# Kernel optimization log

Hardware: AMD Instinct MI355X
Metric: run time of the kernel (lower is better)

Reference implementation:

```python
import jax, jax.numpy as jnp
import numpy as np

NUM_GRAPHS = 128
EPS = 1e-5


def _instance_norm(x, seg, num_seg):
    # Per-graph instance norm over rows grouped by seg (PyG InstanceNorm, affine=False).
    ones = jnp.ones((x.shape[0], 1), x.dtype)
    cnt = jnp.maximum(jax.ops.segment_sum(ones, seg, num_segments=num_seg), 1.0)  # [G,1]
    mean = jax.ops.segment_sum(x, seg, num_segments=num_seg) / cnt               # [G,C]
    xc = x - mean[seg]
    var = jax.ops.segment_sum(xc * xc, seg, num_segments=num_seg) / cnt          # [G,C]
    return xc * jax.lax.rsqrt(var[seg] + EPS)


def setup_inputs() -> dict:
    key = jax.random.key(0)
    ks = jax.random.split(key, 8)
    N, E, H, G = 50000, 800000, 64, NUM_GRAPHS
    emb = jax.random.normal(ks[0], (N, H), dtype=jnp.float32)
    edge_index = jax.random.randint(ks[1], (2, E), 0, N, dtype=jnp.int64)
    batch = jnp.sort(jax.random.randint(ks[2], (N,), 0, G, dtype=jnp.int64))
    s1 = 1.0 / np.sqrt(2 * H)
    s2 = 1.0 / np.sqrt(4 * H)
    s3 = 1.0 / np.sqrt(H)
    return {
        "emb": emb,
        "edge_index": edge_index,
        "batch": batch,
        "W1": jax.random.normal(ks[3], (2 * H, 4 * H), dtype=jnp.float32) * s1,
        "b1": jnp.zeros((4 * H,), jnp.float32),
        "W2": jax.random.normal(ks[4], (4 * H, H), dtype=jnp.float32) * s2,
        "b2": jnp.zeros((H,), jnp.float32),
        "W3": jax.random.normal(ks[5], (H, 1), dtype=jnp.float32) * s3,
        "b3": jnp.zeros((1,), jnp.float32),
    }


def reference(emb, edge_index, batch, W1, b1, W2, b2, W3, b3):
    col, row = edge_index[0], edge_index[1]
    # Gather both endpoint embeddings and concat: [E, 2H]
    f12 = jnp.concatenate([emb[col], emb[row]], axis=-1)
    seg = batch[col]  # graph id per edge
    # MLP([2H, 4H, H, 1]): Linear -> InstanceNorm(batch) -> ReLU (dropout=identity in eval)
    h = jnp.maximum(_instance_norm(f12 @ W1 + b1, seg, NUM_GRAPHS), 0.0)
    h = jnp.maximum(_instance_norm(h @ W2 + b2, seg, NUM_GRAPHS), 0.0)
    att_log_logits = h @ W3 + b3  # [E, 1]
    return att_log_logits
```

## Files before the change

kernel.cpp:

```cpp
#include <hip/hip_runtime.h>
#include <hip/hip_bf16.h>
#include <stdint.h>

#define NG 128
#define EPSI 1e-5f

typedef __attribute__((ext_vector_type(8))) __bf16 bf16x8;
typedef __attribute__((ext_vector_type(4))) float f32x4;

union ABFrag { bf16x8 v; unsigned short u[8]; uint4 q; };
union U8 { uint4 q; unsigned short u[8]; };

__device__ __forceinline__ float b2f(unsigned short u){
  union { unsigned int i; float f; } v; v.i = ((unsigned int)u) << 16; return v.f;
}
__device__ __forceinline__ unsigned short f2b(float f){
  union { float f; unsigned int i; } v; v.f = f;
  unsigned int r = v.i + 0x7fffu + ((v.i >> 16) & 1u);
  return (unsigned short)(r >> 16);
}
__device__ __forceinline__ unsigned int pk2(float lo, float hi){
  unsigned int r;
  asm("v_cvt_pk_bf16_f32 %0, %1, %2" : "=v"(r) : "v"(lo), "v"(hi));
  return r;
}

__global__ void kprep(const float* __restrict__ emb, const float* __restrict__ W1,
                      const float* __restrict__ W2,
                      const int* __restrict__ ei, const int* __restrict__ batch,
                      unsigned short* __restrict__ embb, unsigned short* __restrict__ WcF,
                      unsigned short* __restrict__ W2F, unsigned int* __restrict__ hist,
                      unsigned int* __restrict__ nodeh, int N, int E){
  __shared__ unsigned int h[NG];
  for (int i = threadIdx.x; i < NG; i += 256) h[i] = 0;
  __syncthreads();
  int idx = blockIdx.x * 256 + threadIdx.x;
  int stride = gridDim.x * 256;
  int embCnt4 = N * 16;
  for (int i = idx; i < embCnt4; i += stride){
    float4 v = *(const float4*)(emb + (size_t)i * 4);
    ushort4 o; o.x = f2b(v.x); o.y = f2b(v.y); o.z = f2b(v.z); o.w = f2b(v.w);
    *(ushort4*)(embb + (size_t)i * 4) = o;
  }
  for (int i = idx; i < 32 * 2 * 64 * 8; i += stride){
    int j = i & 7, lane = (i >> 3) & 63, ks = (i >> 9) & 1, tn = i >> 10;
    int quad = lane >> 4, l15 = lane & 15;
    int k = ks * 32 + quad * 8 + j;
    int n = tn * 16 + l15;
    float wv = (n < 256) ? W1[k * 256 + n] : W1[(k + 64) * 256 + (n - 256)];
    WcF[i] = f2b(wv);
  }
  for (int i = idx; i < 4 * 8 * 64 * 8; i += stride){
    int j = i & 7, lane = (i >> 3) & 63, ks = (i >> 9) & 7, w = i >> 12;
    int quad = lane >> 4, l15 = lane & 15;
    W2F[i] = f2b(W2[(ks * 32 + quad * 8 + j) * 64 + w * 16 + l15]);
  }
  for (int e = idx; e < E; e += stride){
    int cn = ei[e];
    atomicAdd(&h[batch[cn]], 1u);
    atomicAdd(&nodeh[cn], 1u);
  }
  __syncthreads();
  for (int i = threadIdx.x; i < NG; i += 256)
    if (h[i]) atomicAdd(&hist[i], h[i]);
}

__global__ void __launch_bounds__(256) kscan(const unsigned int* __restrict__ nodeh,
                      const unsigned int* __restrict__ hist,
                      const int* __restrict__ batch,
                      unsigned int* __restrict__ ncursor,
                      unsigned int* __restrict__ gmeta, int N){
  __shared__ unsigned int sh[3];
  __shared__ unsigned int wtot[4];
  int g = blockIdx.x;
  int t = threadIdx.x;
  unsigned int part = 0;
  for (int i = t; i < g; i += 256) part += (hist[i] + 31u) & ~31u;
  #pragma unroll
  for (int d = 1; d < 64; d <<= 1) part += __shfl_xor(part, d);
  if ((t & 63) == 0) wtot[t >> 6] = part;
  if (t == 64 || t == 65){
    int target = g + (t - 64);
    int lo = 0, hi = N;
    while (lo < hi){ int mid = (lo + hi) >> 1; if (batch[mid] < target) lo = mid + 1; else hi = mid; }
    sh[1 + (t - 64)] = lo;
  }
  __syncthreads();
  if (t == 0){
    unsigned int pb = wtot[0] + wtot[1] + wtot[2] + wtot[3];
    sh[0] = pb;
    gmeta[g] = pb;
    if (g == NG - 1) gmeta[NG] = pb + ((hist[g] + 31u) & ~31u);
  }
  __syncthreads();
  unsigned int run = sh[0];
  int lo = (int)sh[1], hi = (int)sh[2];
  int wid = t >> 6;
  for (int base = lo; base < hi; base += 256){
    int i = base + t;
    unsigned int v = (i < hi) ? nodeh[i] : 0u;
    unsigned int x = v;
    #pragma unroll
    for (int d = 1; d < 64; d <<= 1){
      unsigned int y = __shfl_up(x, d);
      if ((t & 63) >= d) x += y;
    }
    if ((t & 63) == 63) wtot[wid] = x;
    __syncthreads();
    unsigned int woff = 0;
    #pragma unroll
    for (int wb = 0; wb < 4; ++wb) if (wb < wid) woff += wtot[wb];
    if (i < hi) ncursor[i] = run + woff + x - v;
    run += wtot[0] + wtot[1] + wtot[2] + wtot[3];
    __syncthreads();
  }
}

__global__ void kscatter(const int* __restrict__ ei, const int* __restrict__ batch, int E,
                         unsigned int* __restrict__ ncursor, int4* __restrict__ einfo){
  int idx = blockIdx.x * 256 + threadIdx.x;
  for (int e = idx; e < E; e += gridDim.x * 256){
    int cn = ei[e], rn = ei[E + e];
    int g = batch[cn];
    unsigned int p = atomicAdd(&ncursor[cn], 1u);
    einfo[p] = make_int4(cn, rn, g, e);
  }
}

__global__ void kpad(int4* __restrict__ einfo, const unsigned int* __restrict__ hist,
                     const unsigned int* __restrict__ gmeta){
  int g = blockIdx.x;
  unsigned int cnt = hist[g];
  if (!cnt) return;
  unsigned int pe = (cnt + 31u) & ~31u;
  if (cnt == pe) return;
  unsigned int base = gmeta[g];
  int4 e0 = einfo[base]; e0.w = -1;
  for (unsigned int i = cnt + threadIdx.x; i < pe; i += 64)
    einfo[base + i] = e0;
}

__global__ void __launch_bounds__(256) kgemm1(const unsigned short* __restrict__ embb,
    const unsigned short* __restrict__ WcF, const float* __restrict__ b1,
    unsigned short* __restrict__ PQb, int Nn){
  int wave = threadIdx.x >> 6, lane = threadIdx.x & 63;
  int quad = lane >> 4, l15 = lane & 15;
  int tm = blockIdx.x * 4 + wave;
  int tmmax = (Nn + 15) >> 4;
  if (tm >= tmmax) return;
  int m = tm * 16 + l15; if (m >= Nn) m = Nn - 1;
  ABFrag a0, a1;
  a0.q = *(const uint4*)(embb + (size_t)m * 64 + quad * 8);
  a1.q = *(const uint4*)(embb + (size_t)m * 64 + 32 + quad * 8);
  int rowbase = tm * 16 + quad * 4;
  #pragma unroll 4
  for (int tn = 0; tn < 32; ++tn){
    ABFrag b0, b1f;
    b0.q  = *(const uint4*)(WcF + ((size_t)(tn * 2 + 0) * 64 + lane) * 8);
    b1f.q = *(const uint4*)(WcF + ((size_t)(tn * 2 + 1) * 64 + lane) * 8);
    f32x4 acc = {0.f, 0.f, 0.f, 0.f};
    acc = __builtin_amdgcn_mfma_f32_16x16x32_bf16(a0.v, b0.v, acc, 0, 0, 0);
    acc = __builtin_amdgcn_mfma_f32_16x16x32_bf16(a1.v, b1f.v, acc, 0, 0, 0);
    int col = tn * 16 + l15;
    float bias = (col < 256) ? b1[col] : 0.0f;
    #pragma unroll
    for (int r = 0; r < 4; ++r){
      int rowg = rowbase + r;
      if (rowg < Nn) PQb[(size_t)rowg * 512 + col] = f2b(acc[r] + bias);
    }
  }
}

__global__ void __launch_bounds__(256) kstats1(const unsigned short* __restrict__ PQb,
                        const int4* __restrict__ einfo, const unsigned int* __restrict__ gmeta,
                        float* __restrict__ sum1, float* __restrict__ sq1){
  __shared__ float lsum[8][256];
  __shared__ float lsq[8][256];
  int tid = threadIdx.x;
  int EP = (int)gmeta[NG];
  int i0 = blockIdx.x * 512;
  if (i0 >= EP) return;
  for (int i = tid; i < 8 * 256; i += 256){ ((float*)lsum)[i] = 0.f; ((float*)lsq)[i] = 0.f; }
  __syncthreads();
  int i1 = min(EP, i0 + 512);
  int gfirst = einfo[i0].z;
  int eo = tid >> 5;
  int c8 = (tid & 31) * 8;
  float s[8], q[8];
  #pragma unroll
  for (int t = 0; t < 8; ++t){ s[t] = 0.f; q[t] = 0.f; }
  int cur = -1;
  auto flushreg = [&](){
    if (cur >= 0){
      unsigned slot = (unsigned)(cur - gfirst);
      if (slot < 8u){
        #pragma unroll
        for (int t = 0; t < 8; ++t){
          atomicAdd(&lsum[slot][c8 + t], s[t]);
          atomicAdd(&lsq[slot][c8 + t], q[t]);
        }
      } else {
        #pragma unroll
        for (int t = 0; t < 8; ++t){
          atomicAdd(&sum1[cur * 256 + c8 + t], s[t]);
          atomicAdd(&sq1[cur * 256 + c8 + t], q[t]);
        }
      }
      #pragma unroll
      for (int t = 0; t < 8; ++t){ s[t] = 0.f; q[t] = 0.f; }
    }
  };
  auto accum = [&](const U8& pu, const U8& qu){
    #pragma unroll
    for (int t = 0; t < 8; ++t){
      float y = b2f(pu.u[t]) + b2f(qu.u[t]);
      s[t] += y; q[t] += y * y;
    }
  };
  for (int p = i0 + eo; p < i1; p += 32){
    int4 ev0 = einfo[p];
    int pa = p + 8, pb = p + 16, pc = p + 24;
    int4 ev1 = (pa < i1) ? einfo[pa] : make_int4(0, 0, -1, -1);
    int4 ev2 = (pb < i1) ? einfo[pb] : make_int4(0, 0, -1, -1);
    int4 ev3 = (pc < i1) ? einfo[pc] : make_int4(0, 0, -1, -1);
    U8 pu0, qu0, pu1, qu1, pu2, qu2, pu3, qu3;
    pu0.q = *(const uint4*)(PQb + (size_t)ev0.x * 512 + c8);
    qu0.q = *(const uint4*)(PQb + (size_t)ev0.y * 512 + 256 + c8);
    pu1.q = *(const uint4*)(PQb + (size_t)ev1.x * 512 + c8);
    qu1.q = *(const uint4*)(PQb + (size_t)ev1.y * 512 + 256 + c8);
    pu2.q = *(const uint4*)(PQb + (size_t)ev2.x * 512 + c8);
    qu2.q = *(const uint4*)(PQb + (size_t)ev2.y * 512 + 256 + c8);
    pu3.q = *(const uint4*)(PQb + (size_t)ev3.x * 512 + c8);
    qu3.q = *(const uint4*)(PQb + (size_t)ev3.y * 512 + 256 + c8);
    if (ev0.z != cur){ flushreg(); cur = ev0.z; }
    if (ev0.w >= 0) accum(pu0, qu0);
    if (ev1.z >= 0){
      if (ev1.z != cur){ flushreg(); cur = ev1.z; }
      if (ev1.w >= 0) accum(pu1, qu1);
    }
    if (ev2.z >= 0){
      if (ev2.z != cur){ flushreg(); cur = ev2.z; }
      if (ev2.w >= 0) accum(pu2, qu2);
    }
    if (ev3.z >= 0){
      if (ev3.z != cur){ flushreg(); cur = ev3.z; }
      if (ev3.w >= 0) accum(pu3, qu3);
    }
  }
  flushreg();
  __syncthreads();
  for (int i = tid; i < 8 * 256; i += 256){
    int slot = i >> 8, ch = i & 255;
    float vs = lsum[slot][ch], vq = lsq[slot][ch];
    if (vs != 0.f || vq != 0.f){
      int g = gfirst + slot;
      atomicAdd(&sum1[g * 256 + ch], vs);
      atomicAdd(&sq1[g * 256 + ch], vq);
    }
  }
}

__global__ void kfin(const float* __restrict__ sum, const float* __restrict__ sq,
                     const unsigned int* __restrict__ hist,
                     float* __restrict__ meanA, float* __restrict__ rstdA, int C){
  int i = blockIdx.x * blockDim.x + threadIdx.x;
  if (i >= NG * C) return;
  int g = i / C;
  float cnt = fmaxf((float)hist[g], 1.0f);
  float m = sum[i] / cnt;
  float v = sq[i] / cnt - m * m;
  meanA[i] = m;
  rstdA[i] = rsqrtf(fmaxf(v, 0.f) + EPSI);
}

__global__ void __launch_bounds__(256) knorm1(unsigned short* __restrict__ PQb,
    const int* __restrict__ batch, const float* __restrict__ mean1,
    const float* __restrict__ rstd1, int N){
  int idx = blockIdx.x * 256 + threadIdx.x;
  if (idx >= N * 32) return;
  int n = idx >> 5, c8 = (idx & 31) * 8;
  int g = batch[n];
  unsigned short* pp = PQb + (size_t)n * 512 + c8;
  U8 pu; pu.q = *(const uint4*)pp;
  const float* mg = mean1 + g * 256 + c8;
  const float* rg = rstd1 + g * 256 + c8;
  float4 m0 = *(const float4*)mg, m1 = *(const float4*)(mg + 4);
  float4 r0 = *(const float4*)rg, r1 = *(const float4*)(rg + 4);
  U8 o;
  o.q.x = pk2((b2f(pu.u[0]) - m0.x) * r0.x, (b2f(pu.u[1]) - m0.y) * r0.y);
  o.q.y = pk2((b2f(pu.u[2]) - m0.z) * r0.z, (b2f(pu.u[3]) - m0.w) * r0.w);
  o.q.z = pk2((b2f(pu.u[4]) - m1.x) * r1.x, (b2f(pu.u[5]) - m1.y) * r1.y);
  o.q.w = pk2((b2f(pu.u[6]) - m1.z) * r1.z, (b2f(pu.u[7]) - m1.w) * r1.w);
  *(uint4*)pp = o.q;
}

__global__ void __launch_bounds__(256, 5) kmain(const unsigned short* __restrict__ PQb,
    const unsigned short* __restrict__ W2F, const int4* __restrict__ einfo,
    const float* __restrict__ rstd1, const float* __restrict__ b2,
    const unsigned int* __restrict__ hist, const unsigned int* __restrict__ gmeta,
    unsigned short* __restrict__ y2b, float* __restrict__ sum2, float* __restrict__ sq2){
  __shared__ unsigned short Blds[4 * 8 * 64 * 8];
  {
    const uint4* src = (const uint4*)W2F;
    uint4* dst = (uint4*)Blds;
    for (int i = threadIdx.x; i < 2048; i += 256) dst[i] = src[i];
  }
  __syncthreads();
  int wave = threadIdx.x >> 6, lane = threadIdx.x & 63;
  int quad = lane >> 4, l15 = lane & 15;
  float b2v[4];
  #pragma unroll
  for (int cg = 0; cg < 4; ++cg) b2v[cg] = b2[cg * 16 + l15];
  int ntiles = (int)(gmeta[NG] >> 5);
  int nw = gridDim.x * 4;
  for (int t = blockIdx.x * 4 + wave; t < ntiles; t += nw){
    int p0 = t * 32;
    int4 ev0 = einfo[p0 + l15];
    int4 ev1 = einfo[p0 + 16 + l15];
    int g = __builtin_amdgcn_readfirstlane(ev0.z);
    const unsigned short* pp0 = PQb + (size_t)ev0.x * 512 + quad * 8;
    const unsigned short* qq0 = PQb + (size_t)ev0.y * 512 + 256 + quad * 8;
    const unsigned short* pp1 = PQb + (size_t)ev1.x * 512 + quad * 8;
    const unsigned short* qq1 = PQb + (size_t)ev1.y * 512 + 256 + quad * 8;
    const float* rr = rstd1 + g * 256 + quad * 8;
    f32x4 acc[8];
    #pragma unroll
    for (int i = 0; i < 8; ++i){ acc[i][0]=0.f; acc[i][1]=0.f; acc[i][2]=0.f; acc[i][3]=0.f; }
    #pragma unroll 2
    for (int ks = 0; ks < 8; ++ks){
      U8 pu0, qu0, pu1, qu1;
      pu0.q = *(const uint4*)(pp0 + ks * 32);
      qu0.q = *(const uint4*)(qq0 + ks * 32);
      pu1.q = *(const uint4*)(pp1 + ks * 32);
      qu1.q = *(const uint4*)(qq1 + ks * 32);
      float4 ra = *(const float4*)(rr + ks * 32);
      float4 rb = *(const float4*)(rr + ks * 32 + 4);
      ABFrag a0, a1;
      a0.q.x = pk2(fmaxf(0.f, b2f(pu0.u[0]) + b2f(qu0.u[0]) * ra.x),
                   fmaxf(0.f, b2f(pu0.u[1]) + b2f(qu0.u[1]) * ra.y));
      a0.q.y = pk2(fmaxf(0.f, b2f(pu0.u[2]) + b2f(qu0.u[2]) * ra.z),
                   fmaxf(0.f, b2f(pu0.u[3]) + b2f(qu0.u[3]) * ra.w));
      a0.q.z = pk2(fmaxf(0.f, b2f(pu0.u[4]) + b2f(qu0.u[4]) * rb.x),
                   fmaxf(0.f, b2f(pu0.u[5]) + b2f(qu0.u[5]) * rb.y));
      a0.q.w = pk2(fmaxf(0.f, b2f(pu0.u[6]) + b2f(qu0.u[6]) * rb.z),
                   fmaxf(0.f, b2f(pu0.u[7]) + b2f(qu0.u[7]) * rb.w));
      a1.q.x = pk2(fmaxf(0.f, b2f(pu1.u[0]) + b2f(qu1.u[0]) * ra.x),
                   fmaxf(0.f, b2f(pu1.u[1]) + b2f(qu1.u[1]) * ra.y));
      a1.q.y = pk2(fmaxf(0.f, b2f(pu1.u[2]) + b2f(qu1.u[2]) * ra.z),
                   fmaxf(0.f, b2f(pu1.u[3]) + b2f(qu1.u[3]) * ra.w));
      a1.q.z = pk2(fmaxf(0.f, b2f(pu1.u[4]) + b2f(qu1.u[4]) * rb.x),
                   fmaxf(0.f, b2f(pu1.u[5]) + b2f(qu1.u[5]) * rb.y));
      a1.q.w = pk2(fmaxf(0.f, b2f(pu1.u[6]) + b2f(qu1.u[6]) * rb.z),
                   fmaxf(0.f, b2f(pu1.u[7]) + b2f(qu1.u[7]) * rb.w));
      #pragma unroll
      for (int cg = 0; cg < 4; ++cg){
        ABFrag b;
        b.q = *(const uint4*)&Blds[((cg * 8 + ks) * 64 + lane) * 8];
        acc[cg]     = __builtin_amdgcn_mfma_f32_16x16x32_bf16(a0.v, b.v, acc[cg], 0, 0, 0);
        acc[4 + cg] = __builtin_amdgcn_mfma_f32_16x16x32_bf16(a1.v, b.v, acc[4 + cg], 0, 0, 0);
      }
    }
    int nl = (int)gmeta[g] + (int)hist[g] - p0;
    #pragma unroll
    for (int cg = 0; cg < 4; ++cg){
      float s = 0.f, qs = 0.f;
      #pragma unroll
      for (int sub = 0; sub < 2; ++sub)
        #pragma unroll
        for (int r = 0; r < 4; ++r){
          float y = acc[sub * 4 + cg][r] + b2v[cg];
          int el = sub * 16 + quad * 4 + r;
          y2b[(size_t)(p0 + el) * 64 + cg * 16 + l15] = f2b(y);
          if (el < nl){ s += y; qs = fmaf(y, y, qs); }
        }
      s  += __shfl_xor(s, 16);  s  += __shfl_xor(s, 32);
      qs += __shfl_xor(qs, 16); qs += __shfl_xor(qs, 32);
      if (quad == 0){
        atomicAdd(&sum2[g * 64 + cg * 16 + l15], s);
        atomicAdd(&sq2[g * 64 + cg * 16 + l15], qs);
      }
    }
  }
}

__global__ void kfinal(const unsigned short* __restrict__ y2b, const int4* __restrict__ einfo,
                       const unsigned int* __restrict__ gmeta,
                       const float* __restrict__ mean2, const float* __restrict__ rstd2,
                       const float* __restrict__ W3, const float* __restrict__ b3,
                       float* __restrict__ out){
  int EP = (int)gmeta[NG];
  int sub = threadIdx.x & 7;
  int c8 = sub * 8;
  float w3r[8];
  #pragma unroll
  for (int t = 0; t < 8; ++t) w3r[t] = W3[c8 + t];
  float b3v = b3[0];
  int step = (gridDim.x * blockDim.x) >> 3;
  for (int i = (blockIdx.x * blockDim.x + threadIdx.x) >> 3; i < EP; i += step){
    int4 ev = einfo[i];
    U8 yv; yv.q = *(const uint4*)(y2b + (size_t)i * 64 + c8);
    const float* mg = mean2 + ev.z * 64 + c8;
    const float* rg = rstd2 + ev.z * 64 + c8;
    float4 m0 = *(const float4*)mg, m1 = *(const float4*)(mg + 4);
    float4 r0 = *(const float4*)rg, r1 = *(const float4*)(rg + 4);
    float a = 0.f;
    a += fmaxf(0.f, (b2f(yv.u[0]) - m0.x) * r0.x) * w3r[0];
    a += fmaxf(0.f, (b2f(yv.u[1]) - m0.y) * r0.y) * w3r[1];
    a += fmaxf(0.f, (b2f(yv.u[2]) - m0.z) * r0.z) * w3r[2];
    a += fmaxf(0.f, (b2f(yv.u[3]) - m0.w) * r0.w) * w3r[3];
    a += fmaxf(0.f, (b2f(yv.u[4]) - m1.x) * r1.x) * w3r[4];
    a += fmaxf(0.f, (b2f(yv.u[5]) - m1.y) * r1.y) * w3r[5];
    a += fmaxf(0.f, (b2f(yv.u[6]) - m1.z) * r1.z) * w3r[6];
    a += fmaxf(0.f, (b2f(yv.u[7]) - m1.w) * r1.w) * w3r[7];
    a += __shfl_xor(a, 1);
    a += __shfl_xor(a, 2);
    a += __shfl_xor(a, 4);
    if (sub == 0 && ev.w >= 0) out[ev.w] = a + b3v;
  }
}

extern "C" void kernel_launch(void* const* d_in, const int* in_sizes, int n_in,
                              void* d_out, int out_size, void* d_ws, size_t ws_size,
                              hipStream_t stream){
  const float* emb  = (const float*)d_in[0];
  const int*   ei   = (const int*)d_in[1];
  const int*   batch= (const int*)d_in[2];
  const float* W1   = (const float*)d_in[3];
  const float* b1   = (const float*)d_in[4];
  const float* W2   = (const float*)d_in[5];
  const float* b2   = (const float*)d_in[6];
  const float* W3   = (const float*)d_in[7];
  const float* b3   = (const float*)d_in[8];
  int N = in_sizes[0] / 64;
  int E = in_sizes[1] / 2;
  int EPMAX = E + NG * 32;
  float* out = (float*)d_out;

  char* w = (char*)d_ws;
  size_t off = 0;
  auto nxt = [&](size_t bytes) -> char* {
    char* p = w + off;
    off = (off + bytes + 255) & ~(size_t)255;
    return p;
  };
  unsigned short* embb = (unsigned short*)nxt((size_t)N * 64 * 2);
  unsigned short* WcF  = (unsigned short*)nxt(32 * 2 * 64 * 8 * 2);
  unsigned short* W2F  = (unsigned short*)nxt(4 * 8 * 64 * 8 * 2);
  unsigned short* PQb  = (unsigned short*)nxt((size_t)N * 512 * 2);
  unsigned short* y2b  = (unsigned short*)nxt((size_t)EPMAX * 64 * 2);
  int4* einfo = (int4*)nxt((size_t)EPMAX * 16);
  float* mean1 = (float*)nxt(NG * 256 * 4);
  float* rstd1 = (float*)nxt(NG * 256 * 4);
  float* mean2 = (float*)nxt(NG * 64 * 4);
  float* rstd2 = (float*)nxt(NG * 64 * 4);
  unsigned int* ncursor = (unsigned int*)nxt((size_t)N * 4);
  unsigned int* gmeta   = (unsigned int*)nxt((NG + 1) * 4);
  char* zbase = w + off;
  unsigned int* hist  = (unsigned int*)nxt(NG * 4);
  unsigned int* nodeh = (unsigned int*)nxt((size_t)N * 4);
  float* sum1 = (float*)nxt(NG * 256 * 4);
  float* sq1  = (float*)nxt(NG * 256 * 4);
  float* sum2 = (float*)nxt(NG * 64 * 4);
  float* sq2  = (float*)nxt(NG * 64 * 4);
  size_t zbytes = (size_t)((w + off) - zbase);
  hipMemsetAsync(zbase, 0, zbytes, stream);

  kprep<<<2048, 256, 0, stream>>>(emb, W1, W2, ei, batch, embb, WcF, W2F, hist, nodeh, N, E);
  kscan<<<NG, 256, 0, stream>>>(nodeh, hist, batch, ncursor, gmeta, N);
  kscatter<<<2048, 256, 0, stream>>>(ei, batch, E, ncursor, einfo);
  kpad<<<NG, 64, 0, stream>>>(einfo, hist, gmeta);
  {
    int tmmax = (N + 15) / 16;
    kgemm1<<<(tmmax + 3) / 4, 256, 0, stream>>>(embb, WcF, b1, PQb, N);
  }
  kstats1<<<(EPMAX + 511) / 512, 256, 0, stream>>>(PQb, einfo, gmeta, sum1, sq1);
  kfin<<<(NG * 256 + 255) / 256, 256, 0, stream>>>(sum1, sq1, hist, mean1, rstd1, 256);
  knorm1<<<(N * 32 + 255) / 256, 256, 0, stream>>>(PQb, batch, mean1, rstd1, N);
  kmain<<<2048, 256, 0, stream>>>(PQb, W2F, einfo, rstd1, b2, hist, gmeta, y2b, sum2, sq2);
  kfin<<<(NG * 64 + 255) / 256, 256, 0, stream>>>(sum2, sq2, hist, mean2, rstd2, 64);
  kfinal<<<2048, 256, 0, stream>>>(y2b, einfo, gmeta, mean2, rstd2, W3, b3, out);
}
```

Baseline: 505.6 us.

## Restructure layer-1 stats per source node and fold normalization into main kernel

The first-layer statistics kernel now walks source nodes and their outgoing edges. It reads each node's P row once and accumulates only the Q rows of its neighbours, then expands the sums algebraically as cnt*p + S1 and cnt*p^2 + 2p*S1 + S2, which removes the redundant per-edge P gathers. The separate knorm1 pass is dropped: kfin now also emits mean*rstd, and kmain applies (p+q)*rstd - mean*rstd with an fma, saving one full read/write sweep of PQb and a launch. Risks are load imbalance from variable node degree, serialized shuffles per neighbour, and slightly different rounding because p is no longer pre-normalized to bf16.

```diff
diff --git a/kernel.cpp b/kernel.cpp
--- a/kernel.cpp
+++ b/kernel.cpp
@@ -172,84 +172,74 @@
 }
 
 __global__ void __launch_bounds__(256) kstats1(const unsigned short* __restrict__ PQb,
-                        const int4* __restrict__ einfo, const unsigned int* __restrict__ gmeta,
-                        float* __restrict__ sum1, float* __restrict__ sq1){
-  __shared__ float lsum[8][256];
-  __shared__ float lsq[8][256];
+    const int4* __restrict__ einfo, const int* __restrict__ batch,
+    const unsigned int* __restrict__ ncursor, const unsigned int* __restrict__ nodeh,
+    float* __restrict__ sum1, float* __restrict__ sq1, int N){
+  __shared__ float lsum[4][256];
+  __shared__ float lsq[4][256];
   int tid = threadIdx.x;
-  int EP = (int)gmeta[NG];
-  int i0 = blockIdx.x * 512;
-  if (i0 >= EP) return;
-  for (int i = tid; i < 8 * 256; i += 256){ ((float*)lsum)[i] = 0.f; ((float*)lsq)[i] = 0.f; }
-  __syncthreads();
-  int i1 = min(EP, i0 + 512);
-  int gfirst = einfo[i0].z;
-  int eo = tid >> 5;
-  int c8 = (tid & 31) * 8;
-  float s[8], q[8];
-  #pragma unroll
-  for (int t = 0; t < 8; ++t){ s[t] = 0.f; q[t] = 0.f; }
-  int cur = -1;
-  auto flushreg = [&](){
-    if (cur >= 0){
-      unsigned slot = (unsigned)(cur - gfirst);
-      if (slot < 8u){
+  for (int i = tid; i < 4 * 256; i += 256){ ((float*)lsum)[i] = 0.f; ((float*)lsq)[i] = 0.f; }
+  __syncthreads();
+  int base = blockIdx.x * 32;
+  int gfirst = batch[base];
+  int wid = tid >> 6, lane = tid & 63;
+  int c4 = lane * 4;
+  float T1[4] = {0.f,0.f,0.f,0.f}, T2[4] = {0.f,0.f,0.f,0.f};
+  int curg = -1;
+  auto flushT = [&](){
+    if (curg >= 0){
+      unsigned slot = (unsigned)(curg - gfirst);
+      if (slot < 4u){
         #pragma unroll
-        for (int t = 0; t < 8; ++t){
-          atomicAdd(&lsum[slot][c8 + t], s[t]);
-          atomicAdd(&lsq[slot][c8 + t], q[t]);
+        for (int t = 0; t < 4; ++t){
+          atomicAdd(&lsum[slot][c4 + t], T1[t]);
+          atomicAdd(&lsq[slot][c4 + t], T2[t]);
         }
       } else {
         #pragma unroll
-        for (int t = 0; t < 8; ++t){
-          atomicAdd(&sum1[cur * 256 + c8 + t], s[t]);
-          atomicAdd(&sq1[cur * 256 + c8 + t], q[t]);
+        for (int t = 0; t < 4; ++t){
+          atomicAdd(&sum1[curg * 256 + c4 + t], T1[t]);
+          atomicAdd(&sq1[curg * 256 + c4 + t], T2[t]);
         }
       }
       #pragma unroll
-      for (int t = 0; t < 8; ++t){ s[t] = 0.f; q[t] = 0.f; }
+      for (int t = 0; t < 4; ++t){ T1[t] = 0.f; T2[t] = 0.f; }
     }
   };
-  auto accum = [&](const U8& pu, const U8& qu){
-    #pragma unroll
-    for (int t = 0; t < 8; ++t){
-      float y = b2f(pu.u[t]) + b2f(qu.u[t]);
-      s[t] += y; q[t] += y * y;
-    }
-  };
-  for (int p = i0 + eo; p < i1; p += 32){
-    int4 ev0 = einfo[p];
-    int pa = p + 8, pb = p + 16, pc = p + 24;
-    int4 ev1 = (pa < i1) ? einfo[pa] : make_int4(0, 0, -1, -1);
-    int4 ev2 = (pb < i1) ? einfo[pb] : make_int4(0, 0, -1, -1);
-    int4 ev3 = (pc < i1) ? einfo[pc] : make_int4(0, 0, -1, -1);
-    U8 pu0, qu0, pu1, qu1, pu2, qu2, pu3, qu3;
-    pu0.q = *(const uint4*)(PQb + (size_t)ev0.x * 512 + c8);
-    qu0.q = *(const uint4*)(PQb + (size_t)ev0.y * 512 + 256 + c8);
-    pu1.q = *(const uint4*)(PQb + (size_t)ev1.x * 512 + c8);
-    qu1.q = *(const uint4*)(PQb + (size_t)ev1.y * 512 + 256 + c8);
-    pu2.q = *(const uint4*)(PQb + (size_t)ev2.x * 512 + c8);
-    qu2.q = *(const uint4*)(PQb + (size_t)ev2.y * 512 + 256 + c8);
-    pu3.q = *(const uint4*)(PQb + (size_t)ev3.x * 512 + c8);
-    qu3.q = *(const uint4*)(PQb + (size_t)ev3.y * 512 + 256 + c8);
-    if (ev0.z != cur){ flushreg(); cur = ev0.z; }
-    if (ev0.w >= 0) accum(pu0, qu0);
-    if (ev1.z >= 0){
-      if (ev1.z != cur){ flushreg(); cur = ev1.z; }
-      if (ev1.w >= 0) accum(pu1, qu1);
-    }
-    if (ev2.z >= 0){
-      if (ev2.z != cur){ flushreg(); cur = ev2.z; }
-      if (ev2.w >= 0) accum(pu2, qu2);
-    }
-    if (ev3.z >= 0){
-      if (ev3.z != cur){ flushreg(); cur = ev3.z; }
-      if (ev3.w >= 0) accum(pu3, qu3);
-    }
-  }
-  flushreg();
-  __syncthreads();
-  for (int i = tid; i < 8 * 256; i += 256){
+  for (int i = 0; i < 8; ++i){
+    int n = base + wid + i * 4;
+    if (n >= N) break;
+    int g = batch[n];
+    unsigned int cnt = nodeh[n];
+    if (g != curg){ flushT(); curg = g; }
+    if (!cnt) continue;
+    unsigned int start = ncursor[n] - cnt;
+    ushort4 pv = *(const ushort4*)(PQb + (size_t)n * 512 + c4);
+    float S1[4] = {0.f,0.f,0.f,0.f}, S2[4] = {0.f,0.f,0.f,0.f};
+    for (unsigned int jb = 0; jb < cnt; jb += 64){
+      int jn = (int)min(64u, cnt - jb);
+      int rnv = (lane < jn) ? einfo[start + jb + (unsigned)lane].y : 0;
+      #pragma unroll 4
+      for (int j = 0; j < jn; ++j){
+        int rn = __shfl(rnv, j);
+        ushort4 qv = *(const ushort4*)(PQb + (size_t)rn * 512 + 256 + c4);
+        float q0 = b2f(qv.x), q1 = b2f(qv.y), q2 = b2f(qv.z), q3 = b2f(qv.w);
+        S1[0] += q0; S2[0] = fmaf(q0, q0, S2[0]);
+        S1[1] += q1; S2[1] = fmaf(q1, q1, S2[1]);
+        S1[2] += q2; S2[2] = fmaf(q2, q2, S2[2]);
+        S1[3] += q3; S2[3] = fmaf(q3, q3, S2[3]);
+      }
+    }
+    float fc = (float)cnt;
+    float p0 = b2f(pv.x), p1 = b2f(pv.y), p2 = b2f(pv.z), p3 = b2f(pv.w);
+    T1[0] += fmaf(fc, p0, S1[0]);  T2[0] += fmaf(fmaf(fc, p0, 2.f * S1[0]), p0, S2[0]);
+    T1[1] += fmaf(fc, p1, S1[1]);  T2[1] += fmaf(fmaf(fc, p1, 2.f * S1[1]), p1, S2[1]);
+    T1[2] += fmaf(fc, p2, S1[2]);  T2[2] += fmaf(fmaf(fc, p2, 2.f * S1[2]), p2, S2[2]);
+    T1[3] += fmaf(fc, p3, S1[3]);  T2[3] += fmaf(fmaf(fc, p3, 2.f * S1[3]), p3, S2[3]);
+  }
+  flushT();
+  __syncthreads();
+  for (int i = tid; i < 4 * 256; i += 256){
     int slot = i >> 8, ch = i & 255;
     float vs = lsum[slot][ch], vq = lsq[slot][ch];
     if (vs != 0.f || vq != 0.f){
@@ -262,41 +252,24 @@
 
 __global__ void kfin(const float* __restrict__ sum, const float* __restrict__ sq,
                      const unsigned int* __restrict__ hist,
-                     float* __restrict__ meanA, float* __restrict__ rstdA, int C){
+                     float* __restrict__ meanA, float* __restrict__ rstdA,
+                     float* __restrict__ mrA, int C){
   int i = blockIdx.x * blockDim.x + threadIdx.x;
   if (i >= NG * C) return;
   int g = i / C;
   float cnt = fmaxf((float)hist[g], 1.0f);
   float m = sum[i] / cnt;
   float v = sq[i] / cnt - m * m;
+  float r = rsqrtf(fmaxf(v, 0.f) + EPSI);
   meanA[i] = m;
-  rstdA[i] = rsqrtf(fmaxf(v, 0.f) + EPSI);
-}
-
-__global__ void __launch_bounds__(256) knorm1(unsigned short* __restrict__ PQb,
-    const int* __restrict__ batch, const float* __restrict__ mean1,
-    const float* __restrict__ rstd1, int N){
-  int idx = blockIdx.x * 256 + threadIdx.x;
-  if (idx >= N * 32) return;
-  int n = idx >> 5, c8 = (idx & 31) * 8;
-  int g = batch[n];
-  unsigned short* pp = PQb + (size_t)n * 512 + c8;
-  U8 pu; pu.q = *(const uint4*)pp;
-  const float* mg = mean1 + g * 256 + c8;
-  const float* rg = rstd1 + g * 256 + c8;
-  float4 m0 = *(const float4*)mg, m1 = *(const float4*)(mg + 4);
-  float4 r0 = *(const float4*)rg, r1 = *(const float4*)(rg + 4);
-  U8 o;
-  o.q.x = pk2((b2f(pu.u[0]) - m0.x) * r0.x, (b2f(pu.u[1]) - m0.y) * r0.y);
-  o.q.y = pk2((b2f(pu.u[2]) - m0.z) * r0.z, (b2f(pu.u[3]) - m0.w) * r0.w);
-  o.q.z = pk2((b2f(pu.u[4]) - m1.x) * r1.x, (b2f(pu.u[5]) - m1.y) * r1.y);
-  o.q.w = pk2((b2f(pu.u[6]) - m1.z) * r1.z, (b2f(pu.u[7]) - m1.w) * r1.w);
-  *(uint4*)pp = o.q;
+  rstdA[i] = r;
+  mrA[i] = m * r;
 }
 
 __global__ void __launch_bounds__(256, 5) kmain(const unsigned short* __restrict__ PQb,
     const unsigned short* __restrict__ W2F, const int4* __restrict__ einfo,
-    const float* __restrict__ rstd1, const float* __restrict__ b2,
+    const float* __restrict__ rstd1, const float* __restrict__ mr1,
+    const float* __restrict__ b2,
     const unsigned int* __restrict__ hist, const unsigned int* __restrict__ gmeta,
     unsigned short* __restrict__ y2b, float* __restrict__ sum2, float* __restrict__ sq2){
   __shared__ unsigned short Blds[4 * 8 * 64 * 8];
@@ -323,6 +296,7 @@
     const unsigned short* pp1 = PQb + (size_t)ev1.x * 512 + quad * 8;
     const unsigned short* qq1 = PQb + (size_t)ev1.y * 512 + 256 + quad * 8;
     const float* rr = rstd1 + g * 256 + quad * 8;
+    const float* mm = mr1   + g * 256 + quad * 8;
     f32x4 acc[8];
     #pragma unroll
     for (int i = 0; i < 8; ++i){ acc[i][0]=0.f; acc[i][1]=0.f; acc[i][2]=0.f; acc[i][3]=0.f; }
@@ -335,23 +309,33 @@
       qu1.q = *(const uint4*)(qq1 + ks * 32);
       float4 ra = *(const float4*)(rr + ks * 32);
       float4 rb = *(const float4*)(rr + ks * 32 + 4);
+      float4 ma = *(const float4*)(mm + ks * 32);
+      float4 mb = *(const float4*)(mm + ks * 32 + 4);
+      float s00 = b2f(pu0.u[0]) + b2f(qu0.u[0]);
+      float s01 = b2f(pu0.u[1]) + b2f(qu0.u[1]);
+      float s02 = b2f(pu0.u[2]) + b2f(qu0.u[2]);
+      float s03 = b2f(pu0.u[3]) + b2f(qu0.u[3]);
+      float s04 = b2f(pu0.u[4]) + b2f(qu0.u[4]);
+      float s05 = b2f(pu0.u[5]) + b2f(qu0.u[5]);
+      float s06 = b2f(pu0.u[6]) + b2f(qu0.u[6]);
+      float s07 = b2f(pu0.u[7]) + b2f(qu0.u[7]);
+      float s10 = b2f(pu1.u[0]) + b2f(qu1.u[0]);
+      float s11 = b2f(pu1.u[1]) + b2f(qu1.u[1]);
+      float s12 = b2f(pu1.u[2]) + b2f(qu1.u[2]);
+      float s13 = b2f(pu1.u[3]) + b2f(qu1.u[3]);
+      float s14 = b2f(pu1.u[4]) + b2f(qu1.u[4]);
+      float s15 = b2f(pu1.u[5]) + b2f(qu1.u[5]);
+      float s16 = b2f(pu1.u[6]) + b2f(qu1.u[6]);
+      float s17 = b2f(pu1.u[7]) + b2f(qu1.u[7]);
       ABFrag a0, a1;
-      a0.q.x = pk2(fmaxf(0.f, b2f(pu0.u[0]) + b2f(qu0.u[0]) * ra.x),
-                   fmaxf(0.f, b2f(pu0.u[1]) + b2f(qu0.u[1]) * ra.y));
-      a0.q.y = pk2(fmaxf(0.f, b2f(pu0.u[2]) + b2f(qu0.u[2]) * ra.z),
-                   fmaxf(0.f, b2f(pu0.u[3]) + b2f(qu0.u[3]) * ra.w));
-      a0.q.z = pk2(fmaxf(0.f, b2f(pu0.u[4]) + b2f(qu0.u[4]) * rb.x),
-                   fmaxf(0.f, b2f(pu0.u[5]) + b2f(qu0.u[5]) * rb.y));
-      a0.q.w = pk2(fmaxf(0.f, b2f(pu0.u[6]) + b2f(qu0.u[6]) * rb.z),
-                   fmaxf(0.f, b2f(pu0.u[7]) + b2f(qu0.u[7]) * rb.w));
-      a1.q.x = pk2(fmaxf(0.f, b2f(pu1.u[0]) + b2f(qu1.u[0]) * ra.x),
-                   fmaxf(0.f, b2f(pu1.u[1]) + b2f(qu1.u[1]) * ra.y));
-      a1.q.y = pk2(fmaxf(0.f, b2f(pu1.u[2]) + b2f(qu1.u[2]) * ra.z),
-                   fmaxf(0.f, b2f(pu1.u[3]) + b2f(qu1.u[3]) * ra.w));
-      a1.q.z = pk2(fmaxf(0.f, b2f(pu1.u[4]) + b2f(qu1.u[4]) * rb.x),
-                   fmaxf(0.f, b2f(pu1.u[5]) + b2f(qu1.u[5]) * rb.y));
-      a1.q.w = pk2(fmaxf(0.f, b2f(pu1.u[6]) + b2f(qu1.u[6]) * rb.z),
-                   fmaxf(0.f, b2f(pu1.u[7]) + b2f(qu1.u[7]) * rb.w));
+      a0.q.x = pk2(fmaxf(0.f, fmaf(s00, ra.x, -ma.x)), fmaxf(0.f, fmaf(s01, ra.y, -ma.y)));
+      a0.q.y = pk2(fmaxf(0.f, fmaf(s02, ra.z, -ma.z)), fmaxf(0.f, fmaf(s03, ra.w, -ma.w)));
+      a0.q.z = pk2(fmaxf(0.f, fmaf(s04, rb.x, -mb.x)), fmaxf(0.f, fmaf(s05, rb.y, -mb.y)));
+      a0.q.w = pk2(fmaxf(0.f, fmaf(s06, rb.z, -mb.z)), fmaxf(0.f, fmaf(s07, rb.w, -mb.w)));
+      a1.q.x = pk2(fmaxf(0.f, fmaf(s10, ra.x, -ma.x)), fmaxf(0.f, fmaf(s11, ra.y, -ma.y)));
+      a1.q.y = pk2(fmaxf(0.f, fmaf(s12, ra.z, -ma.z)), fmaxf(0.f, fmaf(s13, ra.w, -ma.w)));
+      a1.q.z = pk2(fmaxf(0.f, fmaf(s14, rb.x, -mb.x)), fmaxf(0.f, fmaf(s15, rb.y, -mb.y)));
+      a1.q.w = pk2(fmaxf(0.f, fmaf(s16, rb.z, -mb.z)), fmaxf(0.f, fmaf(s17, rb.w, -mb.w)));
       #pragma unroll
       for (int cg = 0; cg < 4; ++cg){
         ABFrag b;
@@ -451,8 +435,10 @@
   int4* einfo = (int4*)nxt((size_t)EPMAX * 16);
   float* mean1 = (float*)nxt(NG * 256 * 4);
   float* rstd1 = (float*)nxt(NG * 256 * 4);
+  float* mr1   = (float*)nxt(NG * 256 * 4);
   float* mean2 = (float*)nxt(NG * 64 * 4);
   float* rstd2 = (float*)nxt(NG * 64 * 4);
+  float* mr2   = (float*)nxt(NG * 64 * 4);
   unsigned int* ncursor = (unsigned int*)nxt((size_t)N * 4);
   unsigned int* gmeta   = (unsigned int*)nxt((NG + 1) * 4);
   char* zbase = w + off;
@@ -473,10 +459,9 @@
     int tmmax = (N + 15) / 16;
     kgemm1<<<(tmmax + 3) / 4, 256, 0, stream>>>(embb, WcF, b1, PQb, N);
   }
-  kstats1<<<(EPMAX + 511) / 512, 256, 0, stream>>>(PQb, einfo, gmeta, sum1, sq1);
-  kfin<<<(NG * 256 + 255) / 256, 256, 0, stream>>>(sum1, sq1, hist, mean1, rstd1, 256);
-  knorm1<<<(N * 32 + 255) / 256, 256, 0, stream>>>(PQb, batch, mean1, rstd1, N);
-  kmain<<<2048, 256, 0, stream>>>(PQb, W2F, einfo, rstd1, b2, hist, gmeta, y2b, sum2, sq2);
-  kfin<<<(NG * 64 + 255) / 256, 256, 0, stream>>>(sum2, sq2, hist, mean2, rstd2, 64);
+  kstats1<<<(N + 31) / 32, 256, 0, stream>>>(PQb, einfo, batch, ncursor, nodeh, sum1, sq1, N);
+  kfin<<<(NG * 256 + 255) / 256, 256, 0, stream>>>(sum1, sq1, hist, mean1, rstd1, mr1, 256);
+  kmain<<<2048, 256, 0, stream>>>(PQb, W2F, einfo, rstd1, mr1, b2, hist, gmeta, y2b, sum2, sq2);
+  kfin<<<(NG * 64 + 255) / 256, 256, 0, stream>>>(sum2, sq2, hist, mean2, rstd2, mr2, 64);
   kfinal<<<2048, 256, 0, stream>>>(y2b, einfo, gmeta, mean2, rstd2, W3, b3, out);
 }
```

Measured after the change: 519.3 us. 1.03x slower.
